# Optimization experiments

Measured on AMD Instinct MI355X. Metric: run time of the kernel, lower is better.

## Reference

```python
import jax, jax.numpy as jnp
import numpy as np

N, E, G = 10000, 320000, 256
IN_NODE, OUT_NODE, IN_EDGE, HID = 32, 32, 16, 64
BN_EPS = 1e-5


def setup_inputs() -> dict:
    key = jax.random.key(0)
    ks = jax.random.split(key, 8)
    return {
        "x": jax.random.normal(ks[0], (N, IN_NODE), jnp.float32),
        "edge_attr": jax.random.normal(ks[1], (E, IN_EDGE), jnp.float32),
        "edge_index": jax.random.randint(ks[2], (2, E), 0, N),
        "batch": jnp.sort(jax.random.randint(ks[3], (N,), 0, G)),
        "W1": jax.random.normal(ks[4], (IN_EDGE, HID), jnp.float32) * 0.1,
        "b1": jnp.zeros((HID,), jnp.float32),
        "gamma": jnp.ones((HID,), jnp.float32),
        "beta": jnp.zeros((HID,), jnp.float32),
        "W2": jax.random.normal(ks[5], (HID, IN_NODE * OUT_NODE), jnp.float32) * 0.05,
        "b2": jnp.zeros((IN_NODE * OUT_NODE,), jnp.float32),
        "W_root": jax.random.normal(ks[6], (IN_NODE, OUT_NODE), jnp.float32) * 0.1,
        "bias": jnp.zeros((OUT_NODE,), jnp.float32),
        "num_graphs": G,
    }


def reference(x, edge_attr, edge_index, batch, W1, b1, gamma, beta, W2, b2, W_root, bias, num_graphs):
    src, dst = edge_index[0], edge_index[1]
    # edge MLP: Linear -> BatchNorm1d (training-mode batch stats) -> ReLU -> Linear
    h = edge_attr @ W1 + b1                                   # [E, HID]
    mu = jnp.mean(h, axis=0)
    var = jnp.var(h, axis=0)
    h = (h - mu) * jax.lax.rsqrt(var + BN_EPS) * gamma + beta
    h = jax.nn.relu(h)
    w_e = (h @ W2 + b2).reshape(-1, x.shape[1], W_root.shape[1])  # [E, in, out]
    # gather source features, per-edge matmul, scatter-add to targets
    msgs = jnp.einsum('ei,eio->eo', x[src], w_e)              # [E, out]
    aggr = jax.ops.segment_sum(msgs, dst, num_segments=x.shape[0])
    out = aggr + x @ W_root + bias                            # [N, out]
    # global mean pool per graph
    pooled = jax.ops.segment_sum(out, batch, num_segments=num_graphs)
    counts = jax.ops.segment_sum(jnp.ones((x.shape[0],), x.dtype), batch, num_segments=num_graphs)
    return pooled / jnp.maximum(counts, 1.0)[:, None]
```

## Files before the change

### kernel.cpp

```cpp
#include <hip/hip_runtime.h>
#include <stdint.h>

typedef unsigned short u16;
typedef _Float16 f16x2 __attribute__((ext_vector_type(2)));
typedef _Float16 v8h  __attribute__((ext_vector_type(8)));
typedef float    v4f  __attribute__((ext_vector_type(4)));
union U32F16 { uint32_t u; f16x2 h; };
union ABFrag { uint32_t u[4]; v8h h; };

__device__ __forceinline__ float bf2f(u16 v) {
    union { uint32_t u; float f; } c; c.u = ((uint32_t)v) << 16; return c.f;
}
__device__ __forceinline__ u16 f2bf(float f) {
    union { uint32_t u; float f; } c; c.f = f;
    uint32_t u = c.u;
    return (u16)((u + 0x7FFF + ((u >> 16) & 1)) >> 16);
}
__device__ __forceinline__ float loadf(const void* p, size_t i, int isbf) {
    return isbf ? bf2f(((const u16*)p)[i]) : ((const float*)p)[i];
}
__device__ __forceinline__ int get_isbf(const void* gamma) {
    return ((const uint32_t*)gamma)[0] != 0x3F800000u;
}
#define LGKM_WAIT() __asm__ volatile("s_waitcnt lgkmcnt(0)" ::: "memory")

__global__ __launch_bounds__(256) void k_moments(
    const void* __restrict__ ea, const int* __restrict__ eidx,
    float* __restrict__ mom, int* __restrict__ cntn,
    const void* __restrict__ gamma, int E) {
    int isbf = get_isbf(gamma);
    __shared__ float ea_s[128][17];
    int t = threadIdx.x;
    int ii = 0, jj = 0;
    if (t >= 16 && t < 152) {
        int p = t - 16, i2 = 0;
        while (p >= 16 - i2) { p -= 16 - i2; i2++; }
        ii = i2; jj = i2 + p;
    }
    float acc = 0.f;
    int ntiles = (E + 127) >> 7;
    for (int tile = blockIdx.x; tile < ntiles; tile += gridDim.x) {
        int e0 = tile * 128;
        int cnt = min(128, E - e0);
        if (!isbf) {
            for (int u = t; u < 512; u += 256) {
                int el = u >> 2, q = u & 3;
                if (el < cnt) {
                    float4 v = *(const float4*)((const float*)ea + (size_t)(e0 + el) * 16 + q * 4);
                    ea_s[el][q * 4 + 0] = v.x; ea_s[el][q * 4 + 1] = v.y;
                    ea_s[el][q * 4 + 2] = v.z; ea_s[el][q * 4 + 3] = v.w;
                }
            }
        } else {
            int el = t >> 1, q = t & 1;
            if (el < cnt) {
                uint4 v = *(const uint4*)((const u16*)ea + (size_t)(e0 + el) * 16 + q * 8);
                const u16* h8 = (const u16*)&v;
#pragma unroll
                for (int m = 0; m < 8; m++) ea_s[el][q * 8 + m] = bf2f(h8[m]);
            }
        }
        if (t < cnt) atomicAdd(&cntn[eidx[e0 + t]], 1);
        __syncthreads();
        if (t < 16) {
            for (int e = 0; e < cnt; e++) acc += ea_s[e][t];
        } else if (t < 152) {
            for (int e = 0; e < cnt; e++) acc += ea_s[e][ii] * ea_s[e][jj];
        }
        __syncthreads();
    }
    if (t < 152) atomicAdd(&mom[t], acc);
}

__global__ __launch_bounds__(256) void k_scanprep(
    const float* __restrict__ mom,
    const void* __restrict__ W1, const void* __restrict__ b1,
    const void* __restrict__ gamma, const void* __restrict__ beta,
    const int* __restrict__ cntn, int* __restrict__ offsets,
    float* __restrict__ W1eff, float* __restrict__ b1eff, int N, float invE) {
    __shared__ float M[16][16], S[16];
    __shared__ int ssum[256];
    int t = threadIdx.x;
    int isbf = get_isbf(gamma);
    if (t < 16) S[t] = mom[t];
    if (t >= 16 && t < 152) {
        int p = t - 16, i2 = 0;
        while (p >= 16 - i2) { p -= 16 - i2; i2++; }
        float v = mom[t];
        M[i2][i2 + p] = v; M[i2 + p][i2] = v;
    }
    __syncthreads();
    if (t < 64) {
        int k = t;
        float w[16];
#pragma unroll
        for (int i = 0; i < 16; i++) w[i] = loadf(W1, (size_t)i * 64 + k, isbf);
        float s1 = 0.f;
#pragma unroll
        for (int i = 0; i < 16; i++) s1 += w[i] * S[i];
        s1 *= invE;
        float s2 = 0.f;
#pragma unroll
        for (int i = 0; i < 16; i++) {
            float r = 0.f;
#pragma unroll
            for (int j = 0; j < 16; j++) r += w[j] * M[i][j];
            s2 += w[i] * r;
        }
        s2 *= invE;
        float bk = loadf(b1, k, isbf);
        float mu = s1 + bk;
        float var = s2 - s1 * s1;
        float a = loadf(gamma, k, isbf) * rsqrtf(var + 1e-5f);
        b1eff[k] = bk * a + loadf(beta, k, isbf) - mu * a;
#pragma unroll
        for (int i = 0; i < 16; i++) W1eff[i * 64 + k] = w[i] * a;
    }
    int chunk = (N + 255) >> 8;
    int lo = min(t * chunk, N), hi = min(lo + chunk, N);
    int s = 0;
    for (int i = lo; i < hi; i++) s += cntn[i];
    ssum[t] = s; __syncthreads();
    for (int d = 1; d < 256; d <<= 1) {
        int v = (t >= d) ? ssum[t - d] : 0;
        __syncthreads();
        ssum[t] += v;
        __syncthreads();
    }
    int run = ssum[t] - s;
    for (int i = lo; i < hi; i++) { offsets[i] = run; run += cntn[i]; }
    if (t == 255) offsets[N] = run;
}

__global__ __launch_bounds__(256) void k_place(
    const int* __restrict__ eidx, const int* __restrict__ offsets,
    int* __restrict__ cursor, int2* __restrict__ eg,
    const int* __restrict__ batch, int E) {
    int e = blockIdx.x * 256 + threadIdx.x;
    if (e < E) {
        int s = eidx[e];
        int pos = offsets[s] + atomicAdd(&cursor[s], 1);
        int g = batch[eidx[E + e]];
        eg[pos] = make_int2(e, g);
    }
}

__global__ __launch_bounds__(256, 3) void k_nodeQ(
    const void* __restrict__ ea, const int2* __restrict__ eg,
    const void* __restrict__ x, const void* __restrict__ W2, const void* __restrict__ b2,
    const float* __restrict__ W1eff, const float* __restrict__ b1eff,
    const int* __restrict__ offsets, float* __restrict__ pooledA8,
    const void* __restrict__ gamma, int N, int E, int G) {
    __shared__ int offs[5];
    __shared__ float xs[4][32], Rs[4][32];
    __shared__ alignas(16) uint32_t UB[4][1056];
    int t = threadIdx.x;
    int n0 = blockIdx.x * 4;
    if (t < 5) offs[t] = offsets[min(n0 + t, N)];
    int isbf = get_isbf(gamma);
    if (t < 128) {
        int nn = t >> 5, i = t & 31;
        int n = n0 + nn;
        xs[nn][i] = (n < N) ? loadf(x, (size_t)n * 32 + i, isbf) : 0.f;
    }
    __syncthreads();
    if (offs[0] == offs[4]) return;

    {
        int o = t & 31, j2 = t >> 5;
        if (!isbf) {
            const float* W2f = (const float*)W2;
            for (int m = 0; m < 4; m++) {
                int jp = j2 + 8 * m;
                size_t base = (size_t)(2 * jp) * 1024 + o;
                float a[4][2];
#pragma unroll
                for (int nn = 0; nn < 4; nn++) { a[nn][0] = 0.f; a[nn][1] = 0.f; }
#pragma unroll 4
                for (int i = 0; i < 32; i++) {
                    float w0 = W2f[base + i * 32];
                    float w1 = W2f[base + 1024 + i * 32];
#pragma unroll
                    for (int nn = 0; nn < 4; nn++) {
                        float xv = xs[nn][i];
                        a[nn][0] += xv * w0; a[nn][1] += xv * w1;
                    }
                }
#pragma unroll
                for (int nn = 0; nn < 4; nn++) {
                    U32F16 p; p.h.x = (_Float16)a[nn][0]; p.h.y = (_Float16)a[nn][1];
                    UB[nn][jp * 33 + o] = p.u;
                }
            }
        } else {
            const u16* W2h = (const u16*)W2;
            for (int m = 0; m < 4; m++) {
                int jp = j2 + 8 * m;
                size_t base = (size_t)(2 * jp) * 1024 + o;
                float a[4][2];
#pragma unroll
                for (int nn = 0; nn < 4; nn++) { a[nn][0] = 0.f; a[nn][1] = 0.f; }
#pragma unroll 4
                for (int i = 0; i < 32; i++) {
                    float w0 = bf2f(W2h[base + i * 32]);
                    float w1 = bf2f(W2h[base + 1024 + i * 32]);
#pragma unroll
                    for (int nn = 0; nn < 4; nn++) {
                        float xv = xs[nn][i];
                        a[nn][0] += xv * w0; a[nn][1] += xv * w1;
                    }
                }
#pragma unroll
                for (int nn = 0; nn < 4; nn++) {
                    U32F16 p; p.h.x = (_Float16)a[nn][0]; p.h.y = (_Float16)a[nn][1];
                    UB[nn][jp * 33 + o] = p.u;
                }
            }
        }
    }
    if (t < 128) {
        int nn = t >> 5, o = t & 31;
        float acc = 0.f;
#pragma unroll 8
        for (int i = 0; i < 32; i++) acc += xs[nn][i] * loadf(b2, (size_t)i * 32 + o, isbf);
        Rs[nn][o] = acc;
    }
    __syncthreads();

    int w = t >> 6, lane = t & 63;
    int lo = offs[w], hi = offs[w + 1];
    int q = lane >> 4, c = lane & 15;
    int half = lane >> 5, kp = lane & 31;
    uint32_t bfr[2][2][4];
#pragma unroll
    for (int kh = 0; kh < 2; kh++)
#pragma unroll
        for (int oh = 0; oh < 2; oh++)
#pragma unroll
            for (int jj = 0; jj < 4; jj++)
                bfr[kh][oh][jj] = UB[w][(kh * 16 + q * 4 + jj) * 33 + oh * 16 + c];
    float Rv2[2] = { Rs[w][c], Rs[w][16 + c] };
    LGKM_WAIT();
    float*    eaw_w = (float*)&UB[w][0];
    uint32_t* hwb_w = &UB[w][320];
    float w1a[16], w1b[16];
#pragma unroll
    for (int i = 0; i < 16; i++) {
        w1a[i] = W1eff[i * 64 + 2 * kp];
        w1b[i] = W1eff[i * 64 + 2 * kp + 1];
    }
    float bka = b1eff[2 * kp], bkb = b1eff[2 * kp + 1];
    float* poolbase = pooledA8 + (size_t)(blockIdx.x & 7) * G * 32;

    if (lo >= hi) return;

    int2 egc = make_int2(-1, 0), egn = make_int2(-1, 0);
    { int j = lo + (lane & 15); if (lane < 16 && j < hi) egc = eg[j]; }
    { int j = lo + 16 + (lane & 15); if (lane < 16 && j < hi) egn = eg[j]; }
    float4 eaf = make_float4(0, 0, 0, 0);
    uint4  eab = make_uint4(0, 0, 0, 0);
    if (!isbf) {
        int es = __shfl(egc.x, lane >> 2);
        if (es >= 0) eaf = *(const float4*)((const float*)ea + (size_t)es * 16 + (lane & 3) * 4);
    } else {
        int es = __shfl(egc.x, lane >> 1);
        if (lane < 32 && es >= 0) eab = *(const uint4*)((const u16*)ea + (size_t)es * 16 + (lane & 1) * 8);
    }

    for (int j0 = lo; j0 < hi; j0 += 16) {
        int nvalid = min(16, hi - j0);
        if (!isbf) {
            int m = lane >> 2, qq = lane & 3;
            *(float4*)&eaw_w[m * 20 + qq * 4] = eaf;
        } else if (lane < 32) {
            int m = lane >> 1, hh = lane & 1;
            const u16* h8 = (const u16*)&eab;
            float4 f0 = make_float4(bf2f(h8[0]), bf2f(h8[1]), bf2f(h8[2]), bf2f(h8[3]));
            float4 f1 = make_float4(bf2f(h8[4]), bf2f(h8[5]), bf2f(h8[6]), bf2f(h8[7]));
            *(float4*)&eaw_w[m * 20 + hh * 8] = f0;
            *(float4*)&eaw_w[m * 20 + hh * 8 + 4] = f1;
        }
        int2 eg2 = make_int2(-1, 0);
        { int j = j0 + 32 + (lane & 15); if (lane < 16 && j < hi) eg2 = eg[j]; }
        float4 eaf_n = make_float4(0, 0, 0, 0);
        uint4  eab_n = make_uint4(0, 0, 0, 0);
        if (!isbf) {
            int es = __shfl(egn.x, lane >> 2);
            if (es >= 0) eaf_n = *(const float4*)((const float*)ea + (size_t)es * 16 + (lane & 3) * 4);
        } else {
            int es = __shfl(egn.x, lane >> 1);
            if (lane < 32 && es >= 0) eab_n = *(const uint4*)((const u16*)ea + (size_t)es * 16 + (lane & 1) * 8);
        }
        LGKM_WAIT();
#pragma unroll
        for (int m8 = 0; m8 < 8; m8++) {
            int e = half + 2 * m8;
            if (e < nvalid) {
                float ee[16];
                const float4* ep = (const float4*)&eaw_w[e * 20];
                *(float4*)&ee[0] = ep[0]; *(float4*)&ee[4] = ep[1];
                *(float4*)&ee[8] = ep[2]; *(float4*)&ee[12] = ep[3];
                float va = bka, vb = bkb;
#pragma unroll
                for (int i = 0; i < 16; i++) { va += ee[i] * w1a[i]; vb += ee[i] * w1b[i]; }
                U32F16 ph;
                ph.h.x = (_Float16)fmaxf(va, 0.f);
                ph.h.y = (_Float16)fmaxf(vb, 0.f);
                hwb_w[e * 33 + kp] = ph.u;
            }
        }
        LGKM_WAIT();
        ABFrag a0, a1;
#pragma unroll
        for (int jj = 0; jj < 4; jj++) {
            a0.u[jj] = hwb_w[c * 33 + q * 4 + jj];
            a1.u[jj] = hwb_w[c * 33 + 16 + q * 4 + jj];
        }
#pragma unroll
        for (int oh = 0; oh < 2; oh++) {
            ABFrag b0, b1f;
#pragma unroll
            for (int jj = 0; jj < 4; jj++) { b0.u[jj] = bfr[0][oh][jj]; b1f.u[jj] = bfr[1][oh][jj]; }
            v4f d = {0.f, 0.f, 0.f, 0.f};
            d = __builtin_amdgcn_mfma_f32_16x16x32_f16(a0.h, b0.h, d, 0, 0, 0);
            d = __builtin_amdgcn_mfma_f32_16x16x32_f16(a1.h, b1f.h, d, 0, 0, 0);
#pragma unroll
            for (int r = 0; r < 4; r++) {
                int e = q * 4 + r;
                int g = __shfl(egc.y, e);
                if (e < nvalid)
                    atomicAdd(poolbase + (size_t)g * 32 + oh * 16 + c, d[r] + Rv2[oh]);
            }
        }
        egc = egn; egn = eg2; eaf = eaf_n; eab = eab_n;
    }
}

__global__ __launch_bounds__(256) void k_final(
    const float* __restrict__ pooledA8, const void* __restrict__ x,
    const int* __restrict__ batch, const void* __restrict__ Wr,
    const void* __restrict__ bias, void* __restrict__ out,
    const void* __restrict__ gamma, int N, int G) {
    __shared__ float px[8][32];
    __shared__ float Sx[32];
    int g = blockIdx.x;
    int t = threadIdx.x, row = t >> 5, o = t & 31;
    int isbf = get_isbf(gamma);
    int slo = 0, shi = N;
    { int a = 0, b = N; while (a < b) { int m = (a + b) >> 1; if (batch[m] < g) a = m + 1; else b = m; } slo = a; }
    { int a = slo, b = N; while (a < b) { int m = (a + b) >> 1; if (batch[m] < g + 1) a = m + 1; else b = m; } shi = a; }
    float acc = 0.f;
    for (int n = slo + row; n < shi; n += 8) acc += loadf(x, (size_t)n * 32 + o, isbf);
    px[row][o] = acc;
    __syncthreads();
    if (t < 32) {
        float s = 0.f;
#pragma unroll
        for (int r = 0; r < 8; r++) s += px[r][t];
        Sx[t] = s;
    }
    __syncthreads();
    if (t < 32) {
        float v = 0.f;
#pragma unroll
        for (int sh = 0; sh < 8; sh++) v += pooledA8[((size_t)sh * G + g) * 32 + t];
#pragma unroll 8
        for (int i = 0; i < 32; i++) v += Sx[i] * loadf(Wr, (size_t)i * 32 + t, isbf);
        int cnt = shi - slo;
        v += (float)cnt * loadf(bias, t, isbf);
        v /= (float)max(cnt, 1);
        if (isbf) ((u16*)out)[g * 32 + t] = f2bf(v);
        else ((float*)out)[g * 32 + t] = v;
    }
}

extern "C" void kernel_launch(void* const* d_in, const int* in_sizes, int n_in,
                              void* d_out, int out_size, void* d_ws, size_t ws_size,
                              hipStream_t stream) {
    const void* x    = d_in[0];
    const void* ea   = d_in[1];
    const int* eidx  = (const int*)d_in[2];
    const int* batch = (const int*)d_in[3];
    const void* W1   = d_in[4];
    const void* b1   = d_in[5];
    const void* gamma= d_in[6];
    const void* beta = d_in[7];
    const void* W2   = d_in[8];
    const void* b2   = d_in[9];
    const void* Wr   = d_in[10];
    const void* bias = d_in[11];

    int N = in_sizes[0] / 32;
    int E = in_sizes[1] / 16;
    int G = out_size / 32;

    char* ws = (char*)d_ws;
    size_t off = 0;
    auto alloc = [&](size_t bytes) {
        char* p = ws + off;
        off = (off + bytes + 255) & ~(size_t)255;
        return p;
    };
    float* mom      = (float*)alloc(152 * 4);
    float* pooledA8 = (float*)alloc((size_t)8 * G * 32 * 4);
    int*   cntn     = (int*)alloc((size_t)N * 4);
    int*   cursor   = (int*)alloc((size_t)N * 4);
    size_t zero_bytes = off;
    int*   offsets  = (int*)alloc((size_t)(N + 1) * 4);
    int2*  eg       = (int2*)alloc((size_t)E * 8);
    float* W1eff    = (float*)alloc(1024 * 4);
    float* b1eff    = (float*)alloc(64 * 4);
    (void)ws_size; (void)n_in;

    hipMemsetAsync(d_ws, 0, zero_bytes, stream);
    k_moments<<<256, 256, 0, stream>>>(ea, eidx, mom, cntn, gamma, E);
    k_scanprep<<<1, 256, 0, stream>>>(mom, W1, b1, gamma, beta, cntn, offsets,
                                      W1eff, b1eff, N, 1.0f / (float)E);
    k_place<<<(E + 255) / 256, 256, 0, stream>>>(eidx, offsets, cursor, eg, batch, E);
    k_nodeQ<<<(N + 3) / 4, 256, 0, stream>>>(ea, eg, x, W2, b2, W1eff, b1eff,
                                             offsets, pooledA8, gamma, N, E, G);
    k_final<<<G, 256, 0, stream>>>(pooledA8, x, batch, Wr, bias, d_out, gamma, N, G);
}
```

Before: 253.8 us.

## Process 16 nodes per 1024-thread block to amortize W2 reads in node precompute

Grows the node-projection block from 4 nodes/256 threads to 16 nodes/1024 threads. Each thread now computes one output pair for all 16 nodes, reading transposed x from shared memory as float4. This cuts global W2 loads per node by a factor of four. The cost is larger shared memory use (UB grows to 16x1056 words), 32 accumulators per thread, and block-wide syncs over 16 waves, which may lower occupancy and cause more imbalance in the per-node edge loop.

```diff
diff --git a/kernel.cpp b/kernel.cpp
--- a/kernel.cpp
+++ b/kernel.cpp
@@ -145,84 +145,78 @@
     }
 }
 
-__global__ __launch_bounds__(256, 3) void k_nodeQ(
+__global__ __launch_bounds__(1024, 8) void k_nodeQ(
     const void* __restrict__ ea, const int2* __restrict__ eg,
     const void* __restrict__ x, const void* __restrict__ W2, const void* __restrict__ b2,
     const float* __restrict__ W1eff, const float* __restrict__ b1eff,
     const int* __restrict__ offsets, float* __restrict__ pooledA8,
     const void* __restrict__ gamma, int N, int E, int G) {
-    __shared__ int offs[5];
-    __shared__ float xs[4][32], Rs[4][32];
-    __shared__ alignas(16) uint32_t UB[4][1056];
+    __shared__ int offs[17];
+    __shared__ alignas(16) float xsT[32][16];
+    __shared__ float Rs[16][32];
+    __shared__ alignas(16) uint32_t UB[16][1056];
     int t = threadIdx.x;
-    int n0 = blockIdx.x * 4;
-    if (t < 5) offs[t] = offsets[min(n0 + t, N)];
+    int n0 = blockIdx.x * 16;
+    if (t < 17) offs[t] = offsets[min(n0 + t, N)];
     int isbf = get_isbf(gamma);
-    if (t < 128) {
+    if (t < 512) {
         int nn = t >> 5, i = t & 31;
         int n = n0 + nn;
-        xs[nn][i] = (n < N) ? loadf(x, (size_t)n * 32 + i, isbf) : 0.f;
+        xsT[i][nn] = (n < N) ? loadf(x, (size_t)n * 32 + i, isbf) : 0.f;
     }
     __syncthreads();
-    if (offs[0] == offs[4]) return;
+    if (offs[0] == offs[16]) return;
 
     {
-        int o = t & 31, j2 = t >> 5;
+        int o = t & 31, jp = t >> 5;
+        float a0[16], a1[16];
+#pragma unroll
+        for (int nn = 0; nn < 16; nn++) { a0[nn] = 0.f; a1[nn] = 0.f; }
+        size_t base = (size_t)(2 * jp) * 1024 + o;
         if (!isbf) {
             const float* W2f = (const float*)W2;
-            for (int m = 0; m < 4; m++) {
-                int jp = j2 + 8 * m;
-                size_t base = (size_t)(2 * jp) * 1024 + o;
-                float a[4][2];
-#pragma unroll
-                for (int nn = 0; nn < 4; nn++) { a[nn][0] = 0.f; a[nn][1] = 0.f; }
 #pragma unroll 4
-                for (int i = 0; i < 32; i++) {
-                    float w0 = W2f[base + i * 32];
-                    float w1 = W2f[base + 1024 + i * 32];
-#pragma unroll
-                    for (int nn = 0; nn < 4; nn++) {
-                        float xv = xs[nn][i];
-                        a[nn][0] += xv * w0; a[nn][1] += xv * w1;
-                    }
-                }
-#pragma unroll
-                for (int nn = 0; nn < 4; nn++) {
-                    U32F16 p; p.h.x = (_Float16)a[nn][0]; p.h.y = (_Float16)a[nn][1];
-                    UB[nn][jp * 33 + o] = p.u;
+            for (int i = 0; i < 32; i++) {
+                float w0 = W2f[base + (size_t)i * 32];
+                float w1 = W2f[base + 1024 + (size_t)i * 32];
+                const float4* xc = (const float4*)&xsT[i][0];
+#pragma unroll
+                for (int qd = 0; qd < 4; qd++) {
+                    float4 xq = xc[qd];
+                    a0[qd * 4 + 0] += xq.x * w0; a1[qd * 4 + 0] += xq.x * w1;
+                    a0[qd * 4 + 1] += xq.y * w0; a1[qd * 4 + 1] += xq.y * w1;
+                    a0[qd * 4 + 2] += xq.z * w0; a1[qd * 4 + 2] += xq.z * w1;
+                    a0[qd * 4 + 3] += xq.w * w0; a1[qd * 4 + 3] += xq.w * w1;
                 }
             }
         } else {
             const u16* W2h = (const u16*)W2;
-            for (int m = 0; m < 4; m++) {
-                int jp = j2 + 8 * m;
-                size_t base = (size_t)(2 * jp) * 1024 + o;
-                float a[4][2];
-#pragma unroll
-                for (int nn = 0; nn < 4; nn++) { a[nn][0] = 0.f; a[nn][1] = 0.f; }
 #pragma unroll 4
-                for (int i = 0; i < 32; i++) {
-                    float w0 = bf2f(W2h[base + i * 32]);
-                    float w1 = bf2f(W2h[base + 1024 + i * 32]);
-#pragma unroll
-                    for (int nn = 0; nn < 4; nn++) {
-                        float xv = xs[nn][i];
-                        a[nn][0] += xv * w0; a[nn][1] += xv * w1;
-                    }
+            for (int i = 0; i < 32; i++) {
+                float w0 = bf2f(W2h[base + (size_t)i * 32]);
+                float w1 = bf2f(W2h[base + 1024 + (size_t)i * 32]);
+                const float4* xc = (const float4*)&xsT[i][0];
+#pragma unroll
+                for (int qd = 0; qd < 4; qd++) {
+                    float4 xq = xc[qd];
+                    a0[qd * 4 + 0] += xq.x * w0; a1[qd * 4 + 0] += xq.x * w1;
+                    a0[qd * 4 + 1] += xq.y * w0; a1[qd * 4 + 1] += xq.y * w1;
+                    a0[qd * 4 + 2] += xq.z * w0; a1[qd * 4 + 2] += xq.z * w1;
+                    a0[qd * 4 + 3] += xq.w * w0; a1[qd * 4 + 3] += xq.w * w1;
                 }
-#pragma unroll
-                for (int nn = 0; nn < 4; nn++) {
-                    U32F16 p; p.h.x = (_Float16)a[nn][0]; p.h.y = (_Float16)a[nn][1];
-                    UB[nn][jp * 33 + o] = p.u;
-                }
-            }
-        }
-    }
-    if (t < 128) {
+            }
+        }
+#pragma unroll
+        for (int nn = 0; nn < 16; nn++) {
+            U32F16 p; p.h.x = (_Float16)a0[nn]; p.h.y = (_Float16)a1[nn];
+            UB[nn][jp * 33 + o] = p.u;
+        }
+    }
+    if (t < 512) {
         int nn = t >> 5, o = t & 31;
         float acc = 0.f;
 #pragma unroll 8
-        for (int i = 0; i < 32; i++) acc += xs[nn][i] * loadf(b2, (size_t)i * 32 + o, isbf);
+        for (int i = 0; i < 32; i++) acc += xsT[i][nn] * loadf(b2, (size_t)i * 32 + o, isbf);
         Rs[nn][o] = acc;
     }
     __syncthreads();
@@ -310,11 +304,11 @@
             }
         }
         LGKM_WAIT();
-        ABFrag a0, a1;
+        ABFrag a0f, a1f;
 #pragma unroll
         for (int jj = 0; jj < 4; jj++) {
-            a0.u[jj] = hwb_w[c * 33 + q * 4 + jj];
-            a1.u[jj] = hwb_w[c * 33 + 16 + q * 4 + jj];
+            a0f.u[jj] = hwb_w[c * 33 + q * 4 + jj];
+            a1f.u[jj] = hwb_w[c * 33 + 16 + q * 4 + jj];
         }
 #pragma unroll
         for (int oh = 0; oh < 2; oh++) {
@@ -322,8 +316,8 @@
 #pragma unroll
             for (int jj = 0; jj < 4; jj++) { b0.u[jj] = bfr[0][oh][jj]; b1f.u[jj] = bfr[1][oh][jj]; }
             v4f d = {0.f, 0.f, 0.f, 0.f};
-            d = __builtin_amdgcn_mfma_f32_16x16x32_f16(a0.h, b0.h, d, 0, 0, 0);
-            d = __builtin_amdgcn_mfma_f32_16x16x32_f16(a1.h, b1f.h, d, 0, 0, 0);
+            d = __builtin_amdgcn_mfma_f32_16x16x32_f16(a0f.h, b0.h, d, 0, 0, 0);
+            d = __builtin_amdgcn_mfma_f32_16x16x32_f16(a1f.h, b1f.h, d, 0, 0, 0);
 #pragma unroll
             for (int r = 0; r < 4; r++) {
                 int e = q * 4 + r;
@@ -417,7 +411,7 @@
     k_scanprep<<<1, 256, 0, stream>>>(mom, W1, b1, gamma, beta, cntn, offsets,
                                       W1eff, b1eff, N, 1.0f / (float)E);
     k_place<<<(E + 255) / 256, 256, 0, stream>>>(eidx, offsets, cursor, eg, batch, E);
-    k_nodeQ<<<(N + 3) / 4, 256, 0, stream>>>(ea, eg, x, W2, b2, W1eff, b1eff,
-                                             offsets, pooledA8, gamma, N, E, G);
+    k_nodeQ<<<(N + 15) / 16, 1024, 0, stream>>>(ea, eg, x, W2, b2, W1eff, b1eff,
+                                                offsets, pooledA8, gamma, N, E, G);
     k_final<<<G, 256, 0, stream>>>(pooledA8, x, batch, Wr, bias, d_out, gamma, N, G);
 }
```

New measurement: 374.7 us. 47.6% more time.

## Replace per-edge pooled atomics with graph-sorted fp16 message buffer and reduction

Applied to the files above, without the earlier changes.

Instead of atomically adding each edge message into per-graph pooled accumulators, each edge is assigned a slot in a buffer sorted by destination graph (counted and scanned alongside the node offsets). k_nodeQ writes fp16 messages into that buffer, and k_final reduces each graph's contiguous slice. This aims to remove heavy atomic contention on the small pooled array, at the cost of writing and re-reading about 20 MB of messages, extra counting atomics, and fp16 rounding. It falls back to the atomic path when the workspace is too small.

```diff
diff --git a/kernel.cpp b/kernel.cpp
--- a/kernel.cpp
+++ b/kernel.cpp
@@ -16,6 +16,12 @@
     uint32_t u = c.u;
     return (u16)((u + 0x7FFF + ((u >> 16) & 1)) >> 16);
 }
+__device__ __forceinline__ float h16f(u16 v) {
+    union { u16 u; _Float16 h; } c; c.u = v; return (float)c.h;
+}
+__device__ __forceinline__ u16 f16u(float f) {
+    union { _Float16 h; u16 u; } c; c.h = (_Float16)f; return c.u;
+}
 __device__ __forceinline__ float loadf(const void* p, size_t i, int isbf) {
     return isbf ? bf2f(((const u16*)p)[i]) : ((const float*)p)[i];
 }
@@ -26,7 +32,8 @@
 
 __global__ __launch_bounds__(256) void k_moments(
     const void* __restrict__ ea, const int* __restrict__ eidx,
-    float* __restrict__ mom, int* __restrict__ cntn,
+    const int* __restrict__ batch,
+    float* __restrict__ mom, int* __restrict__ cntn, int* __restrict__ gcnt,
     const void* __restrict__ gamma, int E) {
     int isbf = get_isbf(gamma);
     __shared__ float ea_s[128][17];
@@ -60,7 +67,10 @@
                 for (int m = 0; m < 8; m++) ea_s[el][q * 8 + m] = bf2f(h8[m]);
             }
         }
-        if (t < cnt) atomicAdd(&cntn[eidx[e0 + t]], 1);
+        if (t < cnt) {
+            atomicAdd(&cntn[eidx[e0 + t]], 1);
+            atomicAdd(&gcnt[batch[eidx[E + e0 + t]]], 1);
+        }
         __syncthreads();
         if (t < 16) {
             for (int e = 0; e < cnt; e++) acc += ea_s[e][t];
@@ -77,7 +87,9 @@
     const void* __restrict__ W1, const void* __restrict__ b1,
     const void* __restrict__ gamma, const void* __restrict__ beta,
     const int* __restrict__ cntn, int* __restrict__ offsets,
-    float* __restrict__ W1eff, float* __restrict__ b1eff, int N, float invE) {
+    const int* __restrict__ gcnt, int* __restrict__ goff,
+    float* __restrict__ W1eff, float* __restrict__ b1eff,
+    int N, int G, float invE) {
     __shared__ float M[16][16], S[16];
     __shared__ int ssum[256];
     int t = threadIdx.x;
@@ -130,18 +142,35 @@
     int run = ssum[t] - s;
     for (int i = lo; i < hi; i++) { offsets[i] = run; run += cntn[i]; }
     if (t == 255) offsets[N] = run;
+    __syncthreads();
+    int gchunk = (G + 255) >> 8;
+    int glo = min(t * gchunk, G), ghi = min(glo + gchunk, G);
+    int gs = 0;
+    for (int i = glo; i < ghi; i++) gs += gcnt[i];
+    ssum[t] = gs; __syncthreads();
+    for (int d = 1; d < 256; d <<= 1) {
+        int v = (t >= d) ? ssum[t - d] : 0;
+        __syncthreads();
+        ssum[t] += v;
+        __syncthreads();
+    }
+    int grun = ssum[t] - gs;
+    for (int i = glo; i < ghi; i++) { goff[i] = grun; grun += gcnt[i]; }
+    if (t == 255) goff[G] = grun;
 }
 
 __global__ __launch_bounds__(256) void k_place(
     const int* __restrict__ eidx, const int* __restrict__ offsets,
     int* __restrict__ cursor, int2* __restrict__ eg,
-    const int* __restrict__ batch, int E) {
+    const int* __restrict__ batch, const int* __restrict__ goff,
+    int* __restrict__ gcur, int E, int use_msg) {
     int e = blockIdx.x * 256 + threadIdx.x;
     if (e < E) {
         int s = eidx[e];
         int pos = offsets[s] + atomicAdd(&cursor[s], 1);
         int g = batch[eidx[E + e]];
-        eg[pos] = make_int2(e, g);
+        int y = use_msg ? (goff[g] + atomicAdd(&gcur[g], 1)) : g;
+        eg[pos] = make_int2(e, y);
     }
 }
 
@@ -150,6 +179,7 @@
     const void* __restrict__ x, const void* __restrict__ W2, const void* __restrict__ b2,
     const float* __restrict__ W1eff, const float* __restrict__ b1eff,
     const int* __restrict__ offsets, float* __restrict__ pooledA8,
+    u16* __restrict__ msg, int use_msg,
     const void* __restrict__ gamma, int N, int E, int G) {
     __shared__ int offs[5];
     __shared__ float xs[4][32], Rs[4][32];
@@ -324,12 +354,22 @@
             v4f d = {0.f, 0.f, 0.f, 0.f};
             d = __builtin_amdgcn_mfma_f32_16x16x32_f16(a0.h, b0.h, d, 0, 0, 0);
             d = __builtin_amdgcn_mfma_f32_16x16x32_f16(a1.h, b1f.h, d, 0, 0, 0);
-#pragma unroll
-            for (int r = 0; r < 4; r++) {
-                int e = q * 4 + r;
-                int g = __shfl(egc.y, e);
-                if (e < nvalid)
-                    atomicAdd(poolbase + (size_t)g * 32 + oh * 16 + c, d[r] + Rv2[oh]);
+            if (use_msg) {
+#pragma unroll
+                for (int r = 0; r < 4; r++) {
+                    int e = q * 4 + r;
+                    int mp = __shfl(egc.y, e);
+                    if (e < nvalid)
+                        msg[(size_t)mp * 32 + oh * 16 + c] = f16u(d[r] + Rv2[oh]);
+                }
+            } else {
+#pragma unroll
+                for (int r = 0; r < 4; r++) {
+                    int e = q * 4 + r;
+                    int g = __shfl(egc.y, e);
+                    if (e < nvalid)
+                        atomicAdd(poolbase + (size_t)g * 32 + oh * 16 + c, d[r] + Rv2[oh]);
+                }
             }
         }
         egc = egn; egn = eg2; eaf = eaf_n; eab = eab_n;
@@ -337,15 +377,32 @@
 }
 
 __global__ __launch_bounds__(256) void k_final(
-    const float* __restrict__ pooledA8, const void* __restrict__ x,
+    const float* __restrict__ pooledA8, const u16* __restrict__ msg,
+    const int* __restrict__ goff, int use_msg,
+    const void* __restrict__ x,
     const int* __restrict__ batch, const void* __restrict__ Wr,
     const void* __restrict__ bias, void* __restrict__ out,
     const void* __restrict__ gamma, int N, int G) {
     __shared__ float px[8][32];
     __shared__ float Sx[32];
+    __shared__ float ms[256][8];
     int g = blockIdx.x;
     int t = threadIdx.x, row = t >> 5, o = t & 31;
     int isbf = get_isbf(gamma);
+    if (use_msg) {
+        float a8[8];
+#pragma unroll
+        for (int k = 0; k < 8; k++) a8[k] = 0.f;
+        int mlo = goff[g], mhi = goff[g + 1];
+        for (int rr = mlo + (t >> 2); rr < mhi; rr += 64) {
+            uint4 v = *(const uint4*)(msg + (size_t)rr * 32 + (t & 3) * 8);
+            const u16* hp = (const u16*)&v;
+#pragma unroll
+            for (int k = 0; k < 8; k++) a8[k] += h16f(hp[k]);
+        }
+#pragma unroll
+        for (int k = 0; k < 8; k++) ms[t][k] = a8[k];
+    }
     int slo = 0, shi = N;
     { int a = 0, b = N; while (a < b) { int m = (a + b) >> 1; if (batch[m] < g) a = m + 1; else b = m; } slo = a; }
     { int a = slo, b = N; while (a < b) { int m = (a + b) >> 1; if (batch[m] < g + 1) a = m + 1; else b = m; } shi = a; }
@@ -362,8 +419,14 @@
     __syncthreads();
     if (t < 32) {
         float v = 0.f;
-#pragma unroll
-        for (int sh = 0; sh < 8; sh++) v += pooledA8[((size_t)sh * G + g) * 32 + t];
+        if (use_msg) {
+            int quad = t >> 3, k = t & 7;
+#pragma unroll 8
+            for (int j4 = 0; j4 < 64; j4++) v += ms[j4 * 4 + quad][k];
+        } else {
+#pragma unroll
+            for (int sh = 0; sh < 8; sh++) v += pooledA8[((size_t)sh * G + g) * 32 + t];
+        }
 #pragma unroll 8
         for (int i = 0; i < 32; i++) v += Sx[i] * loadf(Wr, (size_t)i * 32 + t, isbf);
         int cnt = shi - slo;
@@ -405,19 +468,27 @@
     float* pooledA8 = (float*)alloc((size_t)8 * G * 32 * 4);
     int*   cntn     = (int*)alloc((size_t)N * 4);
     int*   cursor   = (int*)alloc((size_t)N * 4);
+    int*   gcnt     = (int*)alloc((size_t)G * 4);
+    int*   gcur     = (int*)alloc((size_t)G * 4);
     size_t zero_bytes = off;
     int*   offsets  = (int*)alloc((size_t)(N + 1) * 4);
+    int*   goff     = (int*)alloc((size_t)(G + 1) * 4);
     int2*  eg       = (int2*)alloc((size_t)E * 8);
     float* W1eff    = (float*)alloc(1024 * 4);
     float* b1eff    = (float*)alloc(64 * 4);
-    (void)ws_size; (void)n_in;
+    u16*   msg      = (u16*)alloc((size_t)E * 32 * 2);
+    int use_msg = (off <= ws_size) ? 1 : 0;
+    (void)n_in;
 
     hipMemsetAsync(d_ws, 0, zero_bytes, stream);
-    k_moments<<<256, 256, 0, stream>>>(ea, eidx, mom, cntn, gamma, E);
+    k_moments<<<256, 256, 0, stream>>>(ea, eidx, batch, mom, cntn, gcnt, gamma, E);
     k_scanprep<<<1, 256, 0, stream>>>(mom, W1, b1, gamma, beta, cntn, offsets,
-                                      W1eff, b1eff, N, 1.0f / (float)E);
-    k_place<<<(E + 255) / 256, 256, 0, stream>>>(eidx, offsets, cursor, eg, batch, E);
+                                      gcnt, goff, W1eff, b1eff, N, G, 1.0f / (float)E);
+    k_place<<<(E + 255) / 256, 256, 0, stream>>>(eidx, offsets, cursor, eg, batch,
+                                                 goff, gcur, E, use_msg);
     k_nodeQ<<<(N + 3) / 4, 256, 0, stream>>>(ea, eg, x, W2, b2, W1eff, b1eff,
-                                             offsets, pooledA8, gamma, N, E, G);
-    k_final<<<G, 256, 0, stream>>>(pooledA8, x, batch, Wr, bias, d_out, gamma, N, G);
-}
+                                             offsets, pooledA8, msg, use_msg,
+                                             gamma, N, E, G);
+    k_final<<<G, 256, 0, stream>>>(pooledA8, msg, goff, use_msg, x, batch, Wr, bias,
+                                   d_out, gamma, N, G);
+}
```

Result: slower. 528.0 us (+108.1%).

## Compute edge-attr Gram moments per lane in registers with per-block partials

Applied to the files above, without the earlier changes.

The moments kernel no longer stages 128-edge tiles in shared memory with two barriers per tile, where only 152 of 256 threads did serial sums. Each lane now loads one edge row directly and accumulates half of the upper-triangular Gram matrix plus sums in registers, with wave pairs splitting even and odd rows. Results are reduced with wave shuffles and written as per-block partials rather than global float atomics. The scan-prep kernel then sums 256 partials per entry. The cost is heavy register pressure, about 136 accumulators per lane, which may lower occupancy, plus a serial 256-step reduction in a single-block kernel.

```diff
diff --git a/kernel.cpp b/kernel.cpp
--- a/kernel.cpp
+++ b/kernel.cpp
@@ -24,56 +24,112 @@
 }
 #define LGKM_WAIT() __asm__ volatile("s_waitcnt lgkmcnt(0)" ::: "memory")
 
+template<int P>
+__device__ __forceinline__ void gram_acc(float (&pp)[8][16], float (&s8)[8],
+                                         const float (&v)[16]) {
+#pragma unroll
+    for (int r = 0; r < 8; r++) {
+        const int i = 2 * r + P;
+        const float vi = v[i];
+        s8[r] += vi;
+#pragma unroll
+        for (int j = i; j < 16; j++) pp[r][j] += vi * v[j];
+    }
+}
+#define RED6(s) { s += __shfl_xor(s,1); s += __shfl_xor(s,2); s += __shfl_xor(s,4); \
+                  s += __shfl_xor(s,8); s += __shfl_xor(s,16); s += __shfl_xor(s,32); }
+template<int P>
+__device__ __forceinline__ void gram_flush(float (&pp)[8][16], float (&s8)[8],
+                                           float (*smS)[8], float (*smP)[8][16],
+                                           int wid, int lane) {
+#pragma unroll
+    for (int r = 0; r < 8; r++) {
+        float s = s8[r];
+        RED6(s);
+        if (lane == 0) smS[wid][r] = s;
+#pragma unroll
+        for (int j = 2 * r + P; j < 16; j++) {
+            float q = pp[r][j];
+            RED6(q);
+            if (lane == 0) smP[wid][r][j] = q;
+        }
+    }
+}
+
 __global__ __launch_bounds__(256) void k_moments(
     const void* __restrict__ ea, const int* __restrict__ eidx,
-    float* __restrict__ mom, int* __restrict__ cntn,
+    float* __restrict__ momP, int* __restrict__ cntn,
     const void* __restrict__ gamma, int E) {
     int isbf = get_isbf(gamma);
-    __shared__ float ea_s[128][17];
     int t = threadIdx.x;
-    int ii = 0, jj = 0;
-    if (t >= 16 && t < 152) {
-        int p = t - 16, i2 = 0;
-        while (p >= 16 - i2) { p -= 16 - i2; i2++; }
-        ii = i2; jj = i2 + p;
-    }
-    float acc = 0.f;
-    int ntiles = (E + 127) >> 7;
-    for (int tile = blockIdx.x; tile < ntiles; tile += gridDim.x) {
-        int e0 = tile * 128;
-        int cnt = min(128, E - e0);
+    int lane = t & 63, wid = t >> 6;
+    int p = wid & 1;
+    int team = blockIdx.x * 2 + (wid >> 1);
+    int nteam = gridDim.x * 2;
+    __shared__ float smS[4][8];
+    __shared__ float smP[4][8][16];
+
+    float s8[8];
+    float pp[8][16];
+#pragma unroll
+    for (int r = 0; r < 8; r++) {
+        s8[r] = 0.f;
+#pragma unroll
+        for (int j = 0; j < 16; j++) pp[r][j] = 0.f;
+    }
+
+    for (int b = team * 64; b < E; b += nteam * 64) {
+        int e = b + lane;
+        bool valid = e < E;
+        float v[16];
         if (!isbf) {
-            for (int u = t; u < 512; u += 256) {
-                int el = u >> 2, q = u & 3;
-                if (el < cnt) {
-                    float4 v = *(const float4*)((const float*)ea + (size_t)(e0 + el) * 16 + q * 4);
-                    ea_s[el][q * 4 + 0] = v.x; ea_s[el][q * 4 + 1] = v.y;
-                    ea_s[el][q * 4 + 2] = v.z; ea_s[el][q * 4 + 3] = v.w;
-                }
-            }
+            const float* pe = (const float*)ea + (size_t)e * 16;
+            float4 z = make_float4(0, 0, 0, 0);
+            float4 A = valid ? *(const float4*)(pe + 0)  : z;
+            float4 B = valid ? *(const float4*)(pe + 4)  : z;
+            float4 C = valid ? *(const float4*)(pe + 8)  : z;
+            float4 D = valid ? *(const float4*)(pe + 12) : z;
+            v[0]=A.x; v[1]=A.y; v[2]=A.z; v[3]=A.w;
+            v[4]=B.x; v[5]=B.y; v[6]=B.z; v[7]=B.w;
+            v[8]=C.x; v[9]=C.y; v[10]=C.z; v[11]=C.w;
+            v[12]=D.x; v[13]=D.y; v[14]=D.z; v[15]=D.w;
         } else {
-            int el = t >> 1, q = t & 1;
-            if (el < cnt) {
-                uint4 v = *(const uint4*)((const u16*)ea + (size_t)(e0 + el) * 16 + q * 8);
-                const u16* h8 = (const u16*)&v;
-#pragma unroll
-                for (int m = 0; m < 8; m++) ea_s[el][q * 8 + m] = bf2f(h8[m]);
-            }
-        }
-        if (t < cnt) atomicAdd(&cntn[eidx[e0 + t]], 1);
-        __syncthreads();
+            const u16* ph = (const u16*)ea + (size_t)e * 16;
+            uint4 z = make_uint4(0, 0, 0, 0);
+            uint4 U0 = valid ? *(const uint4*)(ph + 0) : z;
+            uint4 U1 = valid ? *(const uint4*)(ph + 8) : z;
+            const u16* h0 = (const u16*)&U0;
+            const u16* h1 = (const u16*)&U1;
+#pragma unroll
+            for (int m = 0; m < 8; m++) { v[m] = bf2f(h0[m]); v[8 + m] = bf2f(h1[m]); }
+        }
+        if (p == 0) {
+            if (valid) atomicAdd(&cntn[eidx[e]], 1);
+            gram_acc<0>(pp, s8, v);
+        } else {
+            gram_acc<1>(pp, s8, v);
+        }
+    }
+    if (p == 0) gram_flush<0>(pp, s8, smS, smP, wid, lane);
+    else        gram_flush<1>(pp, s8, smS, smP, wid, lane);
+    __syncthreads();
+    if (t < 152) {
+        float val;
         if (t < 16) {
-            for (int e = 0; e < cnt; e++) acc += ea_s[e][t];
-        } else if (t < 152) {
-            for (int e = 0; e < cnt; e++) acc += ea_s[e][ii] * ea_s[e][jj];
-        }
-        __syncthreads();
-    }
-    if (t < 152) atomicAdd(&mom[t], acc);
+            int i = t;
+            val = smS[i & 1][i >> 1] + smS[(i & 1) + 2][i >> 1];
+        } else {
+            int pidx = t - 16, i2 = 0;
+            while (pidx >= 16 - i2) { pidx -= 16 - i2; i2++; }
+            int j = i2 + pidx;
+            val = smP[i2 & 1][i2 >> 1][j] + smP[(i2 & 1) + 2][i2 >> 1][j];
+        }
+        momP[(size_t)blockIdx.x * 152 + t] = val;
+    }
 }
 
 __global__ __launch_bounds__(256) void k_scanprep(
-    const float* __restrict__ mom,
+    const float* __restrict__ momP, int MB,
     const void* __restrict__ W1, const void* __restrict__ b1,
     const void* __restrict__ gamma, const void* __restrict__ beta,
     const int* __restrict__ cntn, int* __restrict__ offsets,
@@ -82,12 +138,16 @@
     __shared__ int ssum[256];
     int t = threadIdx.x;
     int isbf = get_isbf(gamma);
-    if (t < 16) S[t] = mom[t];
+    float mval = 0.f;
+    if (t < 152) {
+#pragma unroll 4
+        for (int b = 0; b < MB; b++) mval += momP[(size_t)b * 152 + t];
+    }
+    if (t < 16) S[t] = mval;
     if (t >= 16 && t < 152) {
         int p = t - 16, i2 = 0;
         while (p >= 16 - i2) { p -= 16 - i2; i2++; }
-        float v = mom[t];
-        M[i2][i2 + p] = v; M[i2 + p][i2] = v;
+        M[i2][i2 + p] = mval; M[i2 + p][i2] = mval;
     }
     __syncthreads();
     if (t < 64) {
@@ -394,6 +454,8 @@
     int E = in_sizes[1] / 16;
     int G = out_size / 32;
 
+    const int MB = 256;
+
     char* ws = (char*)d_ws;
     size_t off = 0;
     auto alloc = [&](size_t bytes) {
@@ -401,11 +463,11 @@
         off = (off + bytes + 255) & ~(size_t)255;
         return p;
     };
-    float* mom      = (float*)alloc(152 * 4);
     float* pooledA8 = (float*)alloc((size_t)8 * G * 32 * 4);
     int*   cntn     = (int*)alloc((size_t)N * 4);
     int*   cursor   = (int*)alloc((size_t)N * 4);
     size_t zero_bytes = off;
+    float* momP     = (float*)alloc((size_t)MB * 152 * 4);
     int*   offsets  = (int*)alloc((size_t)(N + 1) * 4);
     int2*  eg       = (int2*)alloc((size_t)E * 8);
     float* W1eff    = (float*)alloc(1024 * 4);
@@ -413,8 +475,8 @@
     (void)ws_size; (void)n_in;
 
     hipMemsetAsync(d_ws, 0, zero_bytes, stream);
-    k_moments<<<256, 256, 0, stream>>>(ea, eidx, mom, cntn, gamma, E);
-    k_scanprep<<<1, 256, 0, stream>>>(mom, W1, b1, gamma, beta, cntn, offsets,
+    k_moments<<<MB, 256, 0, stream>>>(ea, eidx, momP, cntn, gamma, E);
+    k_scanprep<<<1, 256, 0, stream>>>(momP, MB, W1, b1, gamma, beta, cntn, offsets,
                                       W1eff, b1eff, N, 1.0f / (float)E);
     k_place<<<(E + 255) / 256, 256, 0, stream>>>(eidx, offsets, cursor, eg, batch, E);
     k_nodeQ<<<(N + 3) / 4, 256, 0, stream>>>(ea, eg, x, W2, b2, W1eff, b1eff,
```

Measured after the change: 276.9 us. +9.1%, slower.
